# Performance work log

Hardware: AMD Instinct MI355X
Metric: run time of the kernel (lower is better)

## Reference

```python
import jax, jax.numpy as jnp
import numpy as np

N = 1024
H = 128

def setup_inputs() -> dict:
    key = jax.random.key(0)
    ks = jax.random.split(key, 16)
    s = 1.0 / np.sqrt(H)
    inp = {
        "h": jax.random.normal(ks[0], (N, H), jnp.float32),
        "x": jax.random.normal(ks[1], (N, 2), jnp.float32),
        "batch": jnp.zeros((N,), jnp.int64),
        # Linear params stored as [in, out]
        "Wq": jax.random.normal(ks[2], (H, H), jnp.float32) * s,
        "bq": jnp.zeros((H,), jnp.float32),
        "Wk": jax.random.normal(ks[3], (H, H), jnp.float32) * s,
        "bk": jnp.zeros((H,), jnp.float32),
        "Wv": jax.random.normal(ks[4], (H, H), jnp.float32) * s,
        "bv": jnp.zeros((H,), jnp.float32),
        "We1": jax.random.normal(ks[5], (2, H), jnp.float32) * (1.0 / np.sqrt(2.0)),
        "be1": jnp.zeros((H,), jnp.float32),
        "We2": jax.random.normal(ks[6], (H, H), jnp.float32) * s,
        "be2": jnp.zeros((H,), jnp.float32),
        "Wc": jax.random.normal(ks[7], (H, 1), jnp.float32) * s,
        "bc": jnp.zeros((1,), jnp.float32),
    }
    return inp

def reference(h, x, batch, Wq, bq, Wk, bk, Wv, bv, We1, be1, We2, be2, Wc, bc):
    hidden = h.shape[-1]
    # pairwise relative coordinates: [N, N, 2]
    rel_x = x[:, None, :] - x[None, :, :]
    # edge MLP: Linear(2->H) -> ReLU -> Linear(H->H), [N, N, H]
    edge_feat = jax.nn.relu(rel_x @ We1 + be1) @ We2 + be2
    # attention: scaled dot-product over all pairs
    q = h @ Wq + bq
    k = h @ Wk + bk
    v = h @ Wv + bv
    attn_score = (q @ k.T) / jnp.sqrt(jnp.asarray(hidden, h.dtype))  # [N, N]
    attn_weight = jax.nn.softmax(attn_score, axis=-1)
    agg_h = attn_weight @ v  # [N, H]
    # coordinate update: per-pair scalar gate times rel_x, attn-weighted sum over j
    gate = edge_feat @ Wc + bc                     # [N, N, 1]
    delta_x = jnp.sum(attn_weight[:, :, None] * gate * rel_x, axis=1)  # [N, 2]
    return (h + agg_h, x + delta_x)
```

## Files before the change

kernel.cpp:

```cpp
#include <hip/hip_runtime.h>
#include <math.h>

#define NN 1024
#define HH 128

typedef _Float16 h2 __attribute__((ext_vector_type(2)));
typedef _Float16 h4 __attribute__((ext_vector_type(4)));
typedef _Float16 h8 __attribute__((ext_vector_type(8)));

__device__ inline float fdot2(h2 a, h2 b, float c) {
  return __builtin_amdgcn_fdot2(a, b, c, false);
}

__global__ __launch_bounds__(384) void qkv_kernel(
    const float* __restrict__ h,
    const float* __restrict__ Wq, const float* __restrict__ bq,
    const float* __restrict__ Wk, const float* __restrict__ bk,
    const float* __restrict__ Wv, const float* __restrict__ bv,
    const float* __restrict__ We2, const float* __restrict__ be2,
    const float* __restrict__ Wc, const float* __restrict__ bc,
    float* __restrict__ q, h2* __restrict__ kTp, h2* __restrict__ vp,
    float* __restrict__ Wc2, float* __restrict__ bc2) {
  const int t = threadIdx.x;

  if (blockIdx.x == 256) {
    if (t < HH) {
      float a = 0.f;
      for (int d = 0; d < HH; ++d) a = fmaf(We2[t * HH + d], Wc[d], a);
      Wc2[t] = a;
      if (t == 0) {
        float b = bc[0];
        for (int d = 0; d < HH; ++d) b = fmaf(be2[d], Wc[d], b);
        *bc2 = b;
      }
    }
    return;
  }

  __shared__ float4 hs4[HH];
  const int r0 = blockIdx.x * 4;
  if (t < HH) {
    hs4[t] = make_float4(h[(r0 + 0) * HH + t], h[(r0 + 1) * HH + t],
                         h[(r0 + 2) * HH + t], h[(r0 + 3) * HH + t]);
  }
  __syncthreads();

  const int mat = t >> 7;
  const int col = t & 127;
  const float* W = (mat == 0) ? Wq : (mat == 1) ? Wk : Wv;
  const float* B = (mat == 0) ? bq : (mat == 1) ? bk : bv;
  const float b = B[col];
  float a0 = b, a1 = b, a2 = b, a3 = b;
#pragma unroll 8
  for (int c = 0; c < HH; ++c) {
    float w = W[c * HH + col];
    float4 hv = hs4[c];
    a0 = fmaf(hv.x, w, a0);
    a1 = fmaf(hv.y, w, a1);
    a2 = fmaf(hv.z, w, a2);
    a3 = fmaf(hv.w, w, a3);
  }
  if (mat == 0) {
    q[(r0 + 0) * HH + col] = a0;
    q[(r0 + 1) * HH + col] = a1;
    q[(r0 + 2) * HH + col] = a2;
    q[(r0 + 3) * HH + col] = a3;
  } else if (mat == 1) {
    _Float16* kf = (_Float16*)kTp;
    const int base = ((col >> 1) * NN + r0) * 2 + (col & 1);
    kf[base + 0] = (_Float16)a0;
    kf[base + 2] = (_Float16)a1;
    kf[base + 4] = (_Float16)a2;
    kf[base + 6] = (_Float16)a3;
  } else {
    h2 v01, v23;
    v01.x = (_Float16)a0; v01.y = (_Float16)a1;
    v23.x = (_Float16)a2; v23.y = (_Float16)a3;
    h2* e = vp + ((r0 >> 1) * HH + col);
    e[0] = v01;
    e[HH] = v23;
  }
}

__global__ __launch_bounds__(512) void attn_kernel(
    const float* __restrict__ h, const float* __restrict__ x,
    const float* __restrict__ q, const h2* __restrict__ kTp,
    const h2* __restrict__ vp,
    const float* __restrict__ We1, const float* __restrict__ be1,
    const float* __restrict__ Wc2p, const float* __restrict__ bc2p,
    float* __restrict__ out) {
  __shared__ h8 qpx8[HH / 2];
  __shared__ h8 wcomb[HH / 2];
  __shared__ h4 wsp01[NN / 2];
  __shared__ h4 wsp23[NN / 2];
  __shared__ float xs[NN * 2];
  __shared__ float part[8][4][HH];
  __shared__ float red[12][8];

  const int i0 = blockIdx.x * 4;
  const int tid = threadIdx.x;
  const int lane = tid & 63, wave = tid >> 6;

  if (tid < HH / 2) {
    const int u = tid;
    h8 a, w;
#pragma unroll
    for (int r = 0; r < 4; ++r) {
      a[2 * r] = (_Float16)q[(i0 + r) * HH + 2 * u];
      a[2 * r + 1] = (_Float16)q[(i0 + r) * HH + 2 * u + 1];
    }
    qpx8[u] = a;
    w[0] = (_Float16)We1[2 * u];
    w[1] = (_Float16)We1[2 * u + 1];
    w[2] = (_Float16)We1[HH + 2 * u];
    w[3] = (_Float16)We1[HH + 2 * u + 1];
    w[4] = (_Float16)be1[2 * u];
    w[5] = (_Float16)be1[2 * u + 1];
    w[6] = (_Float16)Wc2p[2 * u];
    w[7] = (_Float16)Wc2p[2 * u + 1];
    wcomb[u] = w;
  }
  for (int j = tid; j < NN * 2; j += 512) xs[j] = x[j];
  const float bc2 = *bc2p;
  __syncthreads();

  const float xjx0 = xs[4 * tid + 0], xjy0 = xs[4 * tid + 1];
  const float xjx1 = xs[4 * tid + 2], xjy1 = xs[4 * tid + 3];
  float rxf[4][2], ryf[4][2];
  h2 RX[4][2], RY[4][2], Z2;
  Z2.x = Z2.y = (_Float16)0;
#pragma unroll
  for (int r = 0; r < 4; ++r) {
    const float xix = xs[2 * (i0 + r)], xiy = xs[2 * (i0 + r) + 1];
    rxf[r][0] = xix - xjx0; ryf[r][0] = xiy - xjy0;
    rxf[r][1] = xix - xjx1; ryf[r][1] = xiy - xjy1;
#pragma unroll
    for (int jj = 0; jj < 2; ++jj) {
      RX[r][jj].x = RX[r][jj].y = (_Float16)rxf[r][jj];
      RY[r][jj].x = RY[r][jj].y = (_Float16)ryf[r][jj];
    }
  }

  float s[4][2] = {}, g[4][2];
#pragma unroll
  for (int r = 0; r < 4; ++r) g[r][0] = g[r][1] = bc2;
  const h4* kT4 = (const h4*)kTp;
#pragma unroll 4
  for (int u = 0; u < HH / 2; ++u) {
    h4 kk = kT4[u * (NN / 2) + tid];
    h8 qq = qpx8[u];
    h8 wc = wcomb[u];
    h2 ka, kb, w0, w1, bb, cc;
    ka.x = kk[0]; ka.y = kk[1];
    kb.x = kk[2]; kb.y = kk[3];
    w0.x = wc[0]; w0.y = wc[1];
    w1.x = wc[2]; w1.y = wc[3];
    bb.x = wc[4]; bb.y = wc[5];
    cc.x = wc[6]; cc.y = wc[7];
#pragma unroll
    for (int r = 0; r < 4; ++r) {
      h2 qr;
      qr.x = qq[2 * r]; qr.y = qq[2 * r + 1];
      s[r][0] = fdot2(qr, ka, s[r][0]);
      s[r][1] = fdot2(qr, kb, s[r][1]);
      h2 t0 = RX[r][0] * w0 + RY[r][0] * w1 + bb;
      h2 t1 = RX[r][1] * w0 + RY[r][1] * w1 + bb;
      t0 = __builtin_elementwise_max(t0, Z2);
      t1 = __builtin_elementwise_max(t1, Z2);
      g[r][0] = fdot2(t0, cc, g[r][0]);
      g[r][1] = fdot2(t1, cc, g[r][1]);
    }
  }
  const float scale = 0.08838834764831845f;
  float e[4][2], l[4], dx[4], dy[4];
#pragma unroll
  for (int r = 0; r < 4; ++r) {
    e[r][0] = __expf(s[r][0] * scale);
    e[r][1] = __expf(s[r][1] * scale);
    l[r] = e[r][0] + e[r][1];
    const float wg0 = e[r][0] * g[r][0], wg1 = e[r][1] * g[r][1];
    dx[r] = fmaf(wg0, rxf[r][0], wg1 * rxf[r][1]);
    dy[r] = fmaf(wg0, ryf[r][0], wg1 * ryf[r][1]);
  }
  {
    h4 wa, wb;
    wa[0] = (_Float16)e[0][0]; wa[1] = (_Float16)e[0][1];
    wa[2] = (_Float16)e[1][0]; wa[3] = (_Float16)e[1][1];
    wb[0] = (_Float16)e[2][0]; wb[1] = (_Float16)e[2][1];
    wb[2] = (_Float16)e[3][0]; wb[3] = (_Float16)e[3][1];
    wsp01[tid] = wa;
    wsp23[tid] = wb;
  }
#pragma unroll
  for (int off = 32; off > 0; off >>= 1) {
#pragma unroll
    for (int r = 0; r < 4; ++r) {
      l[r] += __shfl_down(l[r], off);
      dx[r] += __shfl_down(dx[r], off);
      dy[r] += __shfl_down(dy[r], off);
    }
  }
  if (lane == 0) {
#pragma unroll
    for (int r = 0; r < 4; ++r) {
      red[r][wave] = l[r];
      red[4 + r][wave] = dx[r];
      red[8 + r][wave] = dy[r];
    }
  }
  __syncthreads();
  float inv[4];
#pragma unroll
  for (int r = 0; r < 4; ++r) {
    float sum = 0.f;
#pragma unroll
    for (int w = 0; w < 8; ++w) sum += red[r][w];
    inv[r] = 1.f / sum;
  }
  if (tid < 4) {
    const int r = tid;
    float DX = 0.f, DY = 0.f;
#pragma unroll
    for (int w = 0; w < 8; ++w) { DX += red[4 + r][w]; DY += red[8 + r][w]; }
    out[NN * HH + (i0 + r) * 2 + 0] = xs[2 * (i0 + r)] + DX * inv[r];
    out[NN * HH + (i0 + r) * 2 + 1] = xs[2 * (i0 + r) + 1] + DY * inv[r];
  }

  {
    const int j2b = wave * 64;
    const h4* v4 = (const h4*)vp;
    float acc[4][2] = {};
#pragma unroll 4
    for (int jj = 0; jj < 64; ++jj) {
      const int j2 = j2b + jj;
      h4 vv = v4[j2 * 64 + lane];
      h4 wa = wsp01[j2];
      h4 wb = wsp23[j2];
      h2 v0, v1;
      v0.x = vv[0]; v0.y = vv[1];
      v1.x = vv[2]; v1.y = vv[3];
      h2 w0, w1, w2, w3;
      w0.x = wa[0]; w0.y = wa[1];
      w1.x = wa[2]; w1.y = wa[3];
      w2.x = wb[0]; w2.y = wb[1];
      w3.x = wb[2]; w3.y = wb[3];
      acc[0][0] = fdot2(w0, v0, acc[0][0]);
      acc[0][1] = fdot2(w0, v1, acc[0][1]);
      acc[1][0] = fdot2(w1, v0, acc[1][0]);
      acc[1][1] = fdot2(w1, v1, acc[1][1]);
      acc[2][0] = fdot2(w2, v0, acc[2][0]);
      acc[2][1] = fdot2(w2, v1, acc[2][1]);
      acc[3][0] = fdot2(w3, v0, acc[3][0]);
      acc[3][1] = fdot2(w3, v1, acc[3][1]);
    }
#pragma unroll
    for (int r = 0; r < 4; ++r) {
      part[wave][r][2 * lane] = acc[r][0];
      part[wave][r][2 * lane + 1] = acc[r][1];
    }
  }
  __syncthreads();
  {
    const int r = tid >> 7, c = tid & 127;
    float sacc = 0.f;
#pragma unroll
    for (int gg = 0; gg < 8; ++gg) sacc += part[gg][r][c];
    out[(i0 + r) * HH + c] = h[(i0 + r) * HH + c] + sacc * inv[r];
  }
}

extern "C" void kernel_launch(void* const* d_in, const int* in_sizes, int n_in,
                              void* d_out, int out_size, void* d_ws, size_t ws_size,
                              hipStream_t stream) {
  const float* h   = (const float*)d_in[0];
  const float* x   = (const float*)d_in[1];
  const float* Wq  = (const float*)d_in[3];
  const float* bq  = (const float*)d_in[4];
  const float* Wk  = (const float*)d_in[5];
  const float* bk  = (const float*)d_in[6];
  const float* Wv  = (const float*)d_in[7];
  const float* bv  = (const float*)d_in[8];
  const float* We1 = (const float*)d_in[9];
  const float* be1 = (const float*)d_in[10];
  const float* We2 = (const float*)d_in[11];
  const float* be2 = (const float*)d_in[12];
  const float* Wc  = (const float*)d_in[13];
  const float* bc  = (const float*)d_in[14];
  float* out = (float*)d_out;

  float* wsf = (float*)d_ws;
  float* q   = wsf;
  h2*   kTp  = (h2*)(wsf + NN * HH);
  h2*   vp   = kTp + (HH / 2) * NN;
  float* Wc2 = (float*)(vp + (NN / 2) * HH);
  float* bc2 = Wc2 + HH;

  qkv_kernel<<<257, 384, 0, stream>>>(h, Wq, bq, Wk, bk, Wv, bv, We2, be2, Wc,
                                      bc, q, kTp, vp, Wc2, bc2);
  attn_kernel<<<256, 512, 0, stream>>>(h, x, q, kTp, vp, We1, be1, Wc2, bc2,
                                       out);
}
```

Baseline: 111.2 us.

## Retile attention to two query rows per block with register-prefetched K/V loads

The attention kernel now processes 2 query rows per block across 512 blocks of 256 threads, instead of 4 rows across 256 blocks of 512 threads. Each thread handles 4 key columns using 16-byte K loads and V loads that are software-prefetched one step ahead in registers. Q is now written as fp16 with the softmax scale already folded in, which halves the Q traffic and removes the scale multiply before the exponential. The intent is more blocks and better latency hiding on a GPU with many CUs. In exchange, K and V are re-read twice as often overall, and the last prefetch reads past the end of the K/V buffers into adjacent workspace.

```diff
diff --git a/kernel.cpp b/kernel.cpp
--- a/kernel.cpp
+++ b/kernel.cpp
@@ -11,6 +11,8 @@
 __device__ inline float fdot2(h2 a, h2 b, float c) {
   return __builtin_amdgcn_fdot2(a, b, c, false);
 }
+__device__ inline h2 lo2(h4 v) { h2 r; r.x = v[0]; r.y = v[1]; return r; }
+__device__ inline h2 hi2(h4 v) { h2 r; r.x = v[2]; r.y = v[3]; return r; }
 
 __global__ __launch_bounds__(384) void qkv_kernel(
     const float* __restrict__ h,
@@ -19,7 +21,7 @@
     const float* __restrict__ Wv, const float* __restrict__ bv,
     const float* __restrict__ We2, const float* __restrict__ be2,
     const float* __restrict__ Wc, const float* __restrict__ bc,
-    float* __restrict__ q, h2* __restrict__ kTp, h2* __restrict__ vp,
+    h2* __restrict__ qp, h2* __restrict__ kTp, h2* __restrict__ vp,
     float* __restrict__ Wc2, float* __restrict__ bc2) {
   const int t = threadIdx.x;
 
@@ -61,10 +63,12 @@
     a3 = fmaf(hv.w, w, a3);
   }
   if (mat == 0) {
-    q[(r0 + 0) * HH + col] = a0;
-    q[(r0 + 1) * HH + col] = a1;
-    q[(r0 + 2) * HH + col] = a2;
-    q[(r0 + 3) * HH + col] = a3;
+    const float scale = 0.08838834764831845f;
+    _Float16* qf = (_Float16*)qp;
+    qf[(r0 + 0) * HH + col] = (_Float16)(a0 * scale);
+    qf[(r0 + 1) * HH + col] = (_Float16)(a1 * scale);
+    qf[(r0 + 2) * HH + col] = (_Float16)(a2 * scale);
+    qf[(r0 + 3) * HH + col] = (_Float16)(a3 * scale);
   } else if (mat == 1) {
     _Float16* kf = (_Float16*)kTp;
     const int base = ((col >> 1) * NN + r0) * 2 + (col & 1);
@@ -82,34 +86,31 @@
   }
 }
 
-__global__ __launch_bounds__(512) void attn_kernel(
+__global__ __launch_bounds__(256) void attn_kernel(
     const float* __restrict__ h, const float* __restrict__ x,
-    const float* __restrict__ q, const h2* __restrict__ kTp,
+    const h2* __restrict__ qp, const h2* __restrict__ kTp,
     const h2* __restrict__ vp,
     const float* __restrict__ We1, const float* __restrict__ be1,
     const float* __restrict__ Wc2p, const float* __restrict__ bc2p,
     float* __restrict__ out) {
-  __shared__ h8 qpx8[HH / 2];
+  __shared__ h4 qpx[HH / 2];
   __shared__ h8 wcomb[HH / 2];
-  __shared__ h4 wsp01[NN / 2];
-  __shared__ h4 wsp23[NN / 2];
+  __shared__ h4 wspA[NN / 2];
   __shared__ float xs[NN * 2];
-  __shared__ float part[8][4][HH];
-  __shared__ float red[12][8];
-
-  const int i0 = blockIdx.x * 4;
+  __shared__ float part[4][2][HH];
+  __shared__ float red[6][4];
+
+  const int i0 = blockIdx.x * 2, i1 = i0 + 1;
   const int tid = threadIdx.x;
   const int lane = tid & 63, wave = tid >> 6;
 
   if (tid < HH / 2) {
     const int u = tid;
-    h8 a, w;
-#pragma unroll
-    for (int r = 0; r < 4; ++r) {
-      a[2 * r] = (_Float16)q[(i0 + r) * HH + 2 * u];
-      a[2 * r + 1] = (_Float16)q[(i0 + r) * HH + 2 * u + 1];
-    }
-    qpx8[u] = a;
+    h2 q0 = qp[i0 * (HH / 2) + u], q1 = qp[i1 * (HH / 2) + u];
+    h4 a;
+    a[0] = q0.x; a[1] = q0.y; a[2] = q1.x; a[3] = q1.y;
+    qpx[u] = a;
+    h8 w;
     w[0] = (_Float16)We1[2 * u];
     w[1] = (_Float16)We1[2 * u + 1];
     w[2] = (_Float16)We1[HH + 2 * u];
@@ -120,81 +121,98 @@
     w[7] = (_Float16)Wc2p[2 * u + 1];
     wcomb[u] = w;
   }
-  for (int j = tid; j < NN * 2; j += 512) xs[j] = x[j];
+  for (int j = tid; j < NN * 2; j += 256) xs[j] = x[j];
   const float bc2 = *bc2p;
   __syncthreads();
 
-  const float xjx0 = xs[4 * tid + 0], xjy0 = xs[4 * tid + 1];
-  const float xjx1 = xs[4 * tid + 2], xjy1 = xs[4 * tid + 3];
-  float rxf[4][2], ryf[4][2];
-  h2 RX[4][2], RY[4][2], Z2;
+  float rxf[2][4], ryf[2][4];
+  h2 RX[2][4], RY[2][4], Z2;
   Z2.x = Z2.y = (_Float16)0;
 #pragma unroll
-  for (int r = 0; r < 4; ++r) {
+  for (int r = 0; r < 2; ++r) {
     const float xix = xs[2 * (i0 + r)], xiy = xs[2 * (i0 + r) + 1];
-    rxf[r][0] = xix - xjx0; ryf[r][0] = xiy - xjy0;
-    rxf[r][1] = xix - xjx1; ryf[r][1] = xiy - xjy1;
-#pragma unroll
-    for (int jj = 0; jj < 2; ++jj) {
+#pragma unroll
+    for (int jj = 0; jj < 4; ++jj) {
+      const int j = 4 * tid + jj;
+      rxf[r][jj] = xix - xs[2 * j];
+      ryf[r][jj] = xiy - xs[2 * j + 1];
       RX[r][jj].x = RX[r][jj].y = (_Float16)rxf[r][jj];
       RY[r][jj].x = RY[r][jj].y = (_Float16)ryf[r][jj];
     }
   }
 
-  float s[4][2] = {}, g[4][2];
-#pragma unroll
-  for (int r = 0; r < 4; ++r) g[r][0] = g[r][1] = bc2;
-  const h4* kT4 = (const h4*)kTp;
-#pragma unroll 4
-  for (int u = 0; u < HH / 2; ++u) {
-    h4 kk = kT4[u * (NN / 2) + tid];
-    h8 qq = qpx8[u];
-    h8 wc = wcomb[u];
-    h2 ka, kb, w0, w1, bb, cc;
-    ka.x = kk[0]; ka.y = kk[1];
-    kb.x = kk[2]; kb.y = kk[3];
-    w0.x = wc[0]; w0.y = wc[1];
-    w1.x = wc[2]; w1.y = wc[3];
-    bb.x = wc[4]; bb.y = wc[5];
-    cc.x = wc[6]; cc.y = wc[7];
-#pragma unroll
-    for (int r = 0; r < 4; ++r) {
-      h2 qr;
-      qr.x = qq[2 * r]; qr.y = qq[2 * r + 1];
-      s[r][0] = fdot2(qr, ka, s[r][0]);
-      s[r][1] = fdot2(qr, kb, s[r][1]);
-      h2 t0 = RX[r][0] * w0 + RY[r][0] * w1 + bb;
-      h2 t1 = RX[r][1] * w0 + RY[r][1] * w1 + bb;
-      t0 = __builtin_elementwise_max(t0, Z2);
-      t1 = __builtin_elementwise_max(t1, Z2);
-      g[r][0] = fdot2(t0, cc, g[r][0]);
-      g[r][1] = fdot2(t1, cc, g[r][1]);
-    }
-  }
-  const float scale = 0.08838834764831845f;
-  float e[4][2], l[4], dx[4], dy[4];
-#pragma unroll
-  for (int r = 0; r < 4; ++r) {
-    e[r][0] = __expf(s[r][0] * scale);
-    e[r][1] = __expf(s[r][1] * scale);
-    l[r] = e[r][0] + e[r][1];
-    const float wg0 = e[r][0] * g[r][0], wg1 = e[r][1] * g[r][1];
-    dx[r] = fmaf(wg0, rxf[r][0], wg1 * rxf[r][1]);
-    dy[r] = fmaf(wg0, ryf[r][0], wg1 * ryf[r][1]);
+  float s[2][4] = {}, g[2][4];
+#pragma unroll
+  for (int r = 0; r < 2; ++r)
+#pragma unroll
+    for (int jj = 0; jj < 4; ++jj) g[r][jj] = bc2;
+
+  const h8* kT8 = (const h8*)kTp;
+  h8 pf0 = kT8[0 * 256 + tid];
+  h8 pf1 = kT8[1 * 256 + tid];
+  h8 pf2 = kT8[2 * 256 + tid];
+  h8 pf3 = kT8[3 * 256 + tid];
+  for (int ub = 0; ub < HH / 2; ub += 4) {
+    h8 cur[4] = {pf0, pf1, pf2, pf3};
+    pf0 = kT8[(ub + 4) * 256 + tid];
+    pf1 = kT8[(ub + 5) * 256 + tid];
+    pf2 = kT8[(ub + 6) * 256 + tid];
+    pf3 = kT8[(ub + 7) * 256 + tid];
+#pragma unroll
+    for (int uu = 0; uu < 4; ++uu) {
+      const int u = ub + uu;
+      h8 kk = cur[uu];
+      h4 qq = qpx[u];
+      h8 wc = wcomb[u];
+      h2 q0, q1, w0, w1, bb, cc;
+      q0.x = qq[0]; q0.y = qq[1];
+      q1.x = qq[2]; q1.y = qq[3];
+      w0.x = wc[0]; w0.y = wc[1];
+      w1.x = wc[2]; w1.y = wc[3];
+      bb.x = wc[4]; bb.y = wc[5];
+      cc.x = wc[6]; cc.y = wc[7];
+#pragma unroll
+      for (int jj = 0; jj < 4; ++jj) {
+        h2 kj;
+        kj.x = kk[2 * jj]; kj.y = kk[2 * jj + 1];
+        s[0][jj] = fdot2(q0, kj, s[0][jj]);
+        s[1][jj] = fdot2(q1, kj, s[1][jj]);
+#pragma unroll
+        for (int r = 0; r < 2; ++r) {
+          h2 tt = RX[r][jj] * w0 + RY[r][jj] * w1 + bb;
+          tt = __builtin_elementwise_max(tt, Z2);
+          g[r][jj] = fdot2(tt, cc, g[r][jj]);
+        }
+      }
+    }
+  }
+
+  float e[2][4], l[2], dx[2], dy[2];
+#pragma unroll
+  for (int r = 0; r < 2; ++r) {
+    l[r] = 0.f; dx[r] = 0.f; dy[r] = 0.f;
+#pragma unroll
+    for (int jj = 0; jj < 4; ++jj) {
+      e[r][jj] = __expf(s[r][jj]);
+      l[r] += e[r][jj];
+      const float wg = e[r][jj] * g[r][jj];
+      dx[r] = fmaf(wg, rxf[r][jj], dx[r]);
+      dy[r] = fmaf(wg, ryf[r][jj], dy[r]);
+    }
   }
   {
     h4 wa, wb;
     wa[0] = (_Float16)e[0][0]; wa[1] = (_Float16)e[0][1];
     wa[2] = (_Float16)e[1][0]; wa[3] = (_Float16)e[1][1];
-    wb[0] = (_Float16)e[2][0]; wb[1] = (_Float16)e[2][1];
-    wb[2] = (_Float16)e[3][0]; wb[3] = (_Float16)e[3][1];
-    wsp01[tid] = wa;
-    wsp23[tid] = wb;
+    wb[0] = (_Float16)e[0][2]; wb[1] = (_Float16)e[0][3];
+    wb[2] = (_Float16)e[1][2]; wb[3] = (_Float16)e[1][3];
+    wspA[2 * tid] = wa;
+    wspA[2 * tid + 1] = wb;
   }
 #pragma unroll
   for (int off = 32; off > 0; off >>= 1) {
 #pragma unroll
-    for (int r = 0; r < 4; ++r) {
+    for (int r = 0; r < 2; ++r) {
       l[r] += __shfl_down(l[r], off);
       dx[r] += __shfl_down(dx[r], off);
       dy[r] += __shfl_down(dy[r], off);
@@ -202,59 +220,56 @@
   }
   if (lane == 0) {
 #pragma unroll
-    for (int r = 0; r < 4; ++r) {
+    for (int r = 0; r < 2; ++r) {
       red[r][wave] = l[r];
-      red[4 + r][wave] = dx[r];
-      red[8 + r][wave] = dy[r];
+      red[2 + r][wave] = dx[r];
+      red[4 + r][wave] = dy[r];
     }
   }
   __syncthreads();
-  float inv[4];
-#pragma unroll
-  for (int r = 0; r < 4; ++r) {
-    float sum = 0.f;
-#pragma unroll
-    for (int w = 0; w < 8; ++w) sum += red[r][w];
+  float inv[2];
+#pragma unroll
+  for (int r = 0; r < 2; ++r) {
+    float sum = red[r][0] + red[r][1] + red[r][2] + red[r][3];
     inv[r] = 1.f / sum;
   }
-  if (tid < 4) {
+  if (tid < 2) {
     const int r = tid;
-    float DX = 0.f, DY = 0.f;
-#pragma unroll
-    for (int w = 0; w < 8; ++w) { DX += red[4 + r][w]; DY += red[8 + r][w]; }
+    const float DX = red[2 + r][0] + red[2 + r][1] + red[2 + r][2] + red[2 + r][3];
+    const float DY = red[4 + r][0] + red[4 + r][1] + red[4 + r][2] + red[4 + r][3];
     out[NN * HH + (i0 + r) * 2 + 0] = xs[2 * (i0 + r)] + DX * inv[r];
     out[NN * HH + (i0 + r) * 2 + 1] = xs[2 * (i0 + r) + 1] + DY * inv[r];
   }
 
   {
-    const int j2b = wave * 64;
+    const int j2b = wave * 128;
     const h4* v4 = (const h4*)vp;
-    float acc[4][2] = {};
-#pragma unroll 4
-    for (int jj = 0; jj < 64; ++jj) {
-      const int j2 = j2b + jj;
-      h4 vv = v4[j2 * 64 + lane];
-      h4 wa = wsp01[j2];
-      h4 wb = wsp23[j2];
-      h2 v0, v1;
-      v0.x = vv[0]; v0.y = vv[1];
-      v1.x = vv[2]; v1.y = vv[3];
-      h2 w0, w1, w2, w3;
-      w0.x = wa[0]; w0.y = wa[1];
-      w1.x = wa[2]; w1.y = wa[3];
-      w2.x = wb[0]; w2.y = wb[1];
-      w3.x = wb[2]; w3.y = wb[3];
-      acc[0][0] = fdot2(w0, v0, acc[0][0]);
-      acc[0][1] = fdot2(w0, v1, acc[0][1]);
-      acc[1][0] = fdot2(w1, v0, acc[1][0]);
-      acc[1][1] = fdot2(w1, v1, acc[1][1]);
-      acc[2][0] = fdot2(w2, v0, acc[2][0]);
-      acc[2][1] = fdot2(w2, v1, acc[2][1]);
-      acc[3][0] = fdot2(w3, v0, acc[3][0]);
-      acc[3][1] = fdot2(w3, v1, acc[3][1]);
-    }
-#pragma unroll
-    for (int r = 0; r < 4; ++r) {
+    float acc[2][2] = {};
+    h4 vp0 = v4[(j2b + 0) * 64 + lane];
+    h4 vp1 = v4[(j2b + 1) * 64 + lane];
+    h4 vp2 = v4[(j2b + 2) * 64 + lane];
+    h4 vp3 = v4[(j2b + 3) * 64 + lane];
+    for (int jj = 0; jj < 128; jj += 4) {
+      h4 vcur[4] = {vp0, vp1, vp2, vp3};
+      vp0 = v4[(j2b + jj + 4) * 64 + lane];
+      vp1 = v4[(j2b + jj + 5) * 64 + lane];
+      vp2 = v4[(j2b + jj + 6) * 64 + lane];
+      vp3 = v4[(j2b + jj + 7) * 64 + lane];
+#pragma unroll
+      for (int q = 0; q < 4; ++q) {
+        const int j2 = j2b + jj + q;
+        h4 vv = vcur[q];
+        h4 wj = wspA[j2];
+        h2 v0 = lo2(vv), v1 = hi2(vv);
+        h2 w0 = lo2(wj), w1 = hi2(wj);
+        acc[0][0] = fdot2(w0, v0, acc[0][0]);
+        acc[0][1] = fdot2(w0, v1, acc[0][1]);
+        acc[1][0] = fdot2(w1, v0, acc[1][0]);
+        acc[1][1] = fdot2(w1, v1, acc[1][1]);
+      }
+    }
+#pragma unroll
+    for (int r = 0; r < 2; ++r) {
       part[wave][r][2 * lane] = acc[r][0];
       part[wave][r][2 * lane + 1] = acc[r][1];
     }
@@ -262,9 +277,7 @@
   __syncthreads();
   {
     const int r = tid >> 7, c = tid & 127;
-    float sacc = 0.f;
-#pragma unroll
-    for (int gg = 0; gg < 8; ++gg) sacc += part[gg][r][c];
+    float sacc = part[0][r][c] + part[1][r][c] + part[2][r][c] + part[3][r][c];
     out[(i0 + r) * HH + c] = h[(i0 + r) * HH + c] + sacc * inv[r];
   }
 }
@@ -288,15 +301,15 @@
   const float* bc  = (const float*)d_in[14];
   float* out = (float*)d_out;
 
-  float* wsf = (float*)d_ws;
-  float* q   = wsf;
-  h2*   kTp  = (h2*)(wsf + NN * HH);
-  h2*   vp   = kTp + (HH / 2) * NN;
+  char* wsb = (char*)d_ws;
+  h2*   qp  = (h2*)wsb;
+  h2*   kTp = qp + NN * (HH / 2);
+  h2*   vp  = kTp + (HH / 2) * NN;
   float* Wc2 = (float*)(vp + (NN / 2) * HH);
   float* bc2 = Wc2 + HH;
 
   qkv_kernel<<<257, 384, 0, stream>>>(h, Wq, bq, Wk, bk, Wv, bv, We2, be2, Wc,
-                                      bc, q, kTp, vp, Wc2, bc2);
-  attn_kernel<<<256, 512, 0, stream>>>(h, x, q, kTp, vp, We1, be1, Wc2, bc2,
+                                      bc, qp, kTp, vp, Wc2, bc2);
+  attn_kernel<<<512, 256, 0, stream>>>(h, x, qp, kTp, vp, We1, be1, Wc2, bc2,
                                        out);
 }
```

Result: no change. 110.8 us (-0.4%).
